# Kernel tuning notes

Measured on AMD Instinct MI355X. Metric: run time of the kernel, lower is better.

## Reference

```python
import jax, jax.numpy as jnp
from jax import lax
import numpy as np

EPS = 1e-5

def _quant(w):
    # BitNet-style binarization: sign(w) scaled by mean(|w|), with STE (identity grad)
    alpha = jnp.mean(jnp.abs(w))
    wq = jnp.sign(w) * alpha
    return w + lax.stop_gradient(wq - w)

def _bn(x, gamma, beta, axes):
    mean = jnp.mean(x, axis=axes, keepdims=True)
    var = jnp.var(x, axis=axes, keepdims=True)
    shape = [1] * x.ndim
    shape[1] = x.shape[1]
    return (x - mean) * lax.rsqrt(var + EPS) * gamma.reshape(shape) + beta.reshape(shape)

def _conv(x, w):
    return lax.conv_general_dilated(x, w, window_strides=(1, 1), padding=((1, 1), (1, 1)),
                                    dimension_numbers=('NCHW', 'OIHW', 'NCHW'))

def _maxpool2(x):
    return lax.reduce_window(x, -jnp.inf, lax.max, (1, 1, 2, 2), (1, 1, 2, 2), 'VALID')

def setup_inputs() -> dict:
    key = jax.random.key(0)
    ks = jax.random.split(key, 5)
    return {
        'x': jax.random.normal(ks[0], (1024, 3, 32, 32), jnp.float32),
        'w1': jax.random.normal(ks[1], (64, 3, 3, 3), jnp.float32) * 0.1,
        'g1': jnp.ones((64,), jnp.float32), 'b1': jnp.zeros((64,), jnp.float32),
        'w2': jax.random.normal(ks[2], (128, 64, 3, 3), jnp.float32) * 0.05,
        'g2': jnp.ones((128,), jnp.float32), 'b2': jnp.zeros((128,), jnp.float32),
        'wfc1': jax.random.normal(ks[3], (256, 8192), jnp.float32) * 0.02,
        'g3': jnp.ones((256,), jnp.float32), 'b3': jnp.zeros((256,), jnp.float32),
        'wfc2': jax.random.normal(ks[4], (10, 256), jnp.float32) * 0.1,
    }

def reference(x, w1, g1, b1, w2, g2, b2, wfc1, g3, b3, wfc2):
    h = _conv(x, _quant(w1))                 # [B,64,32,32]
    h = _maxpool2(jax.nn.relu(_bn(h, g1, b1, (0, 2, 3))))  # [B,64,16,16]
    h = _conv(h, _quant(w2))                 # [B,128,16,16]
    h = _maxpool2(jax.nn.relu(_bn(h, g2, b2, (0, 2, 3))))  # [B,128,8,8]
    h = h.reshape(h.shape[0], -1)            # [B,8192]
    h = h @ _quant(wfc1).T                   # [B,256]
    h = jax.nn.relu(_bn(h, g3, b3, (0,)))
    return h @ _quant(wfc2).T                # [B,10]
```

## Files before the change

kernel.cpp:

```cpp
#include <hip/hip_runtime.h>
#include <stdint.h>

typedef unsigned short u16;
typedef unsigned int u32;
typedef __attribute__((ext_vector_type(8))) short s8v;
typedef __attribute__((ext_vector_type(4))) float f4v;
typedef __attribute__((ext_vector_type(8))) u16 u16x8;
typedef __attribute__((ext_vector_type(4))) u16 u16x4;

__device__ __forceinline__ float bf2f(u16 u){
  union { u32 i; float f; } v; v.i = ((u32)u) << 16; return v.f;
}
__device__ __forceinline__ u16 f2bf(float f){
  union { float f; u32 i; } v; v.f = f;
  u32 i = v.i;
  return (u16)((i + 0x7fffu + ((i >> 16) & 1u)) >> 16);
}
__device__ __forceinline__ float sgnf(float w){
  return (w > 0.f) ? 1.f : ((w < 0.f) ? -1.f : 0.f);
}
__device__ __forceinline__ u16 sgn_bf(float w){
  return (w > 0.f) ? (u16)0x3F80 : ((w < 0.f) ? (u16)0xBF80 : (u16)0);
}

#define GLL16(gaddr, laddr) __builtin_amdgcn_global_load_lds( \
    (const __attribute__((address_space(1))) void*)(gaddr),   \
    (__attribute__((address_space(3))) void*)(laddr), 16, 0, 0)

__global__ __launch_bounds__(256) void k_gen(const float* __restrict__ w1, const float* __restrict__ w2,
                                             const float* __restrict__ wfc2, const float* __restrict__ wfc1,
                                             u16* __restrict__ qw1b, u16* __restrict__ qw2b,
                                             float* __restrict__ qwfc2, u16* __restrict__ qfc1b,
                                             float* __restrict__ partials){
  __shared__ u16 tile[128*72];
  int t = threadIdx.x;
  if (blockIdx.x < 306){
    int i = blockIdx.x * 256 + t;
    float av = 0.f; int slot;
    if (i < 73728){
      int j = i & 7, lane = (i >> 3) & 63, fid = i >> 9;
      int s = fid >> 4, ks = (fid >> 3) & 1, nt = fid & 7;
      int co = (lane & 15)*8 + nt;
      int c = ks*32 + (lane >> 4)*8 + j;
      float wv = w2[((size_t)co*64 + c)*9 + s];
      qw2b[i] = sgn_bf(wv);
      av = fabsf(wv); slot = 1;
    } else if (i < 73728 + 2048){
      int i3 = i - 73728;
      int j = i3 & 7, lane = (i3 >> 3) & 63, nt = i3 >> 9;
      int co = nt*16 + (lane & 15);
      int k = (lane >> 4)*8 + j;
      if (k < 27){
        float wv = w1[co*27 + k];
        qw1b[i3] = sgn_bf(wv);
        av = fabsf(wv);
      } else qw1b[i3] = (u16)0;
      slot = 0;
    } else {
      int i4 = i - (73728 + 2048);
      float wv = wfc2[i4];
      qwfc2[i4] = sgnf(wv);
      av = fabsf(wv); slot = 3;
    }
    #pragma unroll
    for (int off = 32; off > 0; off >>= 1) av += __shfl_xor(av, off);
    if ((t & 63) == 0) atomicAdd(partials + slot*256 + (blockIdx.x & 255), av);
  } else {
    int co = blockIdx.x - 306;
    const float4* src = (const float4*)(wfc1 + (size_t)co*8192);
    float av = 0.f;
    #pragma unroll
    for (int p = 0; p < 8; ++p){
      int k4 = t + p*256;
      float4 v = src[k4];
      int c = k4 >> 4, px = (k4 & 15)*4;
      u16* d = tile + c*72 + px;
      d[0] = sgn_bf(v.x); d[1] = sgn_bf(v.y); d[2] = sgn_bf(v.z); d[3] = sgn_bf(v.w);
      av += fabsf(v.x) + fabsf(v.y) + fabsf(v.z) + fabsf(v.w);
    }
    #pragma unroll
    for (int off = 32; off > 0; off >>= 1) av += __shfl_xor(av, off);
    if ((t & 63) == 0) atomicAdd(partials + 2*256 + (co & 255), av);
    __syncthreads();
    int co4 = co >> 4, co15 = co & 15;
    #pragma unroll
    for (int p = 0; p < 4; ++p){
      int m = t + p*256;
      int px = m >> 4, jj = m & 15;
      int kstep = px*4 + (jj >> 2), l16 = jj & 3;
      u16x8 o;
      #pragma unroll
      for (int u = 0; u < 8; ++u) o[u] = tile[(jj*8 + u)*72 + px];
      *(u16x8*)(qfc1b + ((size_t)(kstep*16 + co4)*512 + (l16*16 + co15)*8)) = o;
    }
  }
}

__global__ void k_red4(const float* __restrict__ partials, float* __restrict__ absum){
  int t = threadIdx.x, w = t >> 6, lane = t & 63;
  const float* p = partials + w*256;
  float s = p[lane] + p[lane + 64] + p[lane + 128] + p[lane + 192];
  #pragma unroll
  for (int off = 32; off > 0; off >>= 1) s += __shfl_xor(s, off);
  if (lane == 0) absum[w] = s;
}

__global__ __launch_bounds__(256) void k_conv1m(const float* __restrict__ x, const u16* __restrict__ qw1b,
                                                const float* __restrict__ absum, u16* __restrict__ p1raw,
                                                float* __restrict__ gs, float* __restrict__ gq){
  __shared__ __align__(8) u16 xs[3*34*36];
  __shared__ float ls1[64], ls2[64];
  int n = blockIdx.x, t = threadIdx.x;
  if (t < 64){ ls1[t] = 0.f; ls2[t] = 0.f; }
  for (int i = t; i < 1836; i += 256) ((u32*)xs)[i] = 0u;
  __syncthreads();
  const float4* xg = (const float4*)(x + (size_t)n * 3072);
  for (int i = t; i < 768; i += 256){
    float4 v = xg[i];
    int ci = i >> 8, rem = i & 255, y = rem >> 3, xq = (rem & 7) * 4;
    int base = ci*1224 + (y+1)*36 + 2 + xq;
    *(u32*)(xs + base)     = (u32)f2bf(v.x) | ((u32)f2bf(v.y) << 16);
    *(u32*)(xs + base + 2) = (u32)f2bf(v.z) | ((u32)f2bf(v.w) << 16);
  }
  int w = t >> 6, lane = t & 63, l15 = lane & 15, q = lane >> 4;
  int koff[8]; u32 kmsk[8];
  #pragma unroll
  for (int j = 0; j < 8; ++j){
    int k = q*8 + j;
    int d9 = (k*57) >> 9;
    int r9 = k - d9*9;
    int d3 = (r9*11) >> 5;
    int r3 = r9 - d3*3;
    koff[j] = d9*1224 + d3*36 + r3;
    kmsk[j] = (k < 27) ? 0xffffu : 0u;
  }
  const s8v* bp = (const s8v*)qw1b;
  s8v bf[4];
  #pragma unroll
  for (int nt = 0; nt < 4; ++nt) bf[nt] = bp[nt*64 + lane];
  float alpha = absum[0] * (1.f/1728.f);
  u16* p1img = p1raw + (size_t)n * 16384;
  float s1v[4], s2v[4];
  #pragma unroll
  for (int nt = 0; nt < 4; ++nt){ s1v[nt] = 0.f; s2v[nt] = 0.f; }
  __syncthreads();
  for (int chunk = 0; chunk < 4; ++chunk){
    #pragma unroll
    for (int i = 0; i < 4; ++i){
      int tl = w*4 + i;
      int r = tl*16 + l15;
      int g = (chunk*256 + r) >> 2, s = r & 3;
      int iy = 2*(g >> 4) + (s >> 1), ix = 2*(g & 15) + (s & 1);
      const u16* xb = xs + iy*36 + ix + 1;
      u32 pk2[4];
      #pragma unroll
      for (int kk = 0; kk < 4; ++kk){
        u32 lo = (u32)xb[koff[2*kk]]     & kmsk[2*kk];
        u32 hi = (u32)xb[koff[2*kk + 1]] & kmsk[2*kk + 1];
        pk2[kk] = lo | (hi << 16);
      }
      s8v av;
      ((u32*)&av)[0] = pk2[0]; ((u32*)&av)[1] = pk2[1];
      ((u32*)&av)[2] = pk2[2]; ((u32*)&av)[3] = pk2[3];
      int go = chunk*64 + tl*4 + q;
      u16* drow = p1img + go*64 + l15;
      #pragma unroll
      for (int nt = 0; nt < 4; ++nt){
        f4v c = (f4v)(0.0f);
        c = __builtin_amdgcn_mfma_f32_16x16x32_bf16(av, bf[nt], c, 0, 0, 0);
        s1v[nt] += c[0] + c[1] + c[2] + c[3];
        s2v[nt] += c[0]*c[0] + c[1]*c[1] + c[2]*c[2] + c[3]*c[3];
        float pm = fmaxf(fmaxf(c[0], c[1]), fmaxf(c[2], c[3]));
        drow[nt*16] = f2bf(pm * alpha);
      }
    }
  }
  #pragma unroll
  for (int nt = 0; nt < 4; ++nt){
    s1v[nt] += __shfl_xor(s1v[nt], 16); s1v[nt] += __shfl_xor(s1v[nt], 32);
    s2v[nt] += __shfl_xor(s2v[nt], 16); s2v[nt] += __shfl_xor(s2v[nt], 32);
  }
  if (q == 0){
    #pragma unroll
    for (int nt = 0; nt < 4; ++nt){
      atomicAdd(&ls1[nt*16 + l15], s1v[nt]);
      atomicAdd(&ls2[nt*16 + l15], s2v[nt]);
    }
  }
  __syncthreads();
  if (t < 64){
    atomicAdd(gs + t, ls1[t] * alpha);
    atomicAdd(gq + t, ls2[t] * alpha * alpha);
  }
}

__global__ __launch_bounds__(512, 4) void k_conv2m(const u16* __restrict__ p1raw, const u16* __restrict__ qw2b,
                                                   const float* __restrict__ absum,
                                                   const float* __restrict__ s1, const float* __restrict__ q1,
                                                   const float* __restrict__ g1, const float* __restrict__ b1,
                                                   u16* __restrict__ p2raw,
                                                   float* __restrict__ gs, float* __restrict__ gq){
  __shared__ __align__(16) u16 img[288*64];
  __shared__ __align__(16) u16 bstage[3][4096];
  int n = blockIdx.x, t = threadIdx.x;
  int c0 = (t & 7) * 8;
  float scv[8], biv[8];
  #pragma unroll
  for (int j = 0; j < 8; ++j){
    float m = s1[c0+j] * (1.f/1048576.f);
    float var = q1[c0+j] * (1.f/1048576.f) - m*m;
    float sc = g1[c0+j] * rsqrtf(var + 1e-5f);
    scv[j] = sc; biv[j] = b1[c0+j] - m*sc;
  }
  if (t < 256){
    int cl = t >> 7, y = (t >> 3) & 15, unit = t & 7;
    int px = y*18 + cl*17;
    int su = unit ^ (px & 7);
    *(u16x8*)(img + px*64 + su*8) = (u16x8)(u16)0;
  }
  const u16* src = p1raw + (size_t)n * 16384;
  #pragma unroll
  for (int i = 0; i < 4; ++i){
    int id = i*512 + t;
    int p0 = id >> 3, unit = id & 7;
    int y = p0 >> 4, xq = p0 & 15;
    int px = y*18 + xq + 1;
    int su = unit ^ (px & 7);
    u16x8 v = *(const u16x8*)(src + id*8);
    u16x8 o;
    #pragma unroll
    for (int j = 0; j < 8; ++j)
      o[j] = f2bf(fmaxf(bf2f(v[j]) * scv[j] + biv[j], 0.f));
    *(u16x8*)(img + px*64 + su*8) = o;
  }
  int w = t >> 6, lane = t & 63, l15 = lane & 15, q = lane >> 4;
  int wr = w >> 1, wc = w & 1;
  const char* bsrc = (const char*)qw2b;
  {
    const char* g = bsrc + w*1024 + lane*16;
    char* l = ((char*)bstage[0]) + w*1024;
    GLL16(g, l);
  }
  __syncthreads();
  f4v acc[4][4];
  #pragma unroll
  for (int a = 0; a < 4; ++a)
    #pragma unroll
    for (int b = 0; b < 4; ++b) acc[a][b] = (f4v)(0.0f);
  for (int p = 0; p < 18; ++p){
    int s = p >> 1, ks = p & 1;
    int dy = s / 3, dx = s - dy*3;
    if (p < 17){
      const char* g = bsrc + (size_t)(p + 1)*8192 + w*1024 + lane*16;
      char* l = ((char*)bstage[(p + 1) % 3]) + w*1024;
      GLL16(g, l);
      asm volatile("s_waitcnt vmcnt(1)" ::: "memory");
    } else {
      asm volatile("s_waitcnt vmcnt(0)" ::: "memory");
    }
    __builtin_amdgcn_s_barrier();
    asm volatile("" ::: "memory");
    const u16* bb = bstage[p % 3];
    s8v bf[4];
    #pragma unroll
    for (int nt = 0; nt < 4; ++nt) bf[nt] = *(const s8v*)(bb + ((wc*4 + nt)*64 + lane)*8);
    __builtin_amdgcn_s_setprio(1);
    #pragma unroll
    for (int mt = 0; mt < 4; ++mt){
      int yv = wr*4 + mt + dy - 1;
      if (yv >= 0 && yv <= 15){
        int px = yv*18 + l15 + dx;
        int su = (ks*4 + q) ^ (px & 7);
        s8v av = *(const s8v*)(img + px*64 + su*8);
        #pragma unroll
        for (int nt = 0; nt < 4; ++nt)
          acc[mt][nt] = __builtin_amdgcn_mfma_f32_16x16x32_bf16(av, bf[nt], acc[mt][nt], 0, 0, 0);
      }
    }
    __builtin_amdgcn_s_setprio(0);
  }
  float alpha = absum[1] * (1.f/73728.f);
  float s1v[4], s2v[4];
  #pragma unroll
  for (int nt = 0; nt < 4; ++nt){ s1v[nt] = 0.f; s2v[nt] = 0.f; }
  #pragma unroll
  for (int mp = 0; mp < 2; ++mp){
    #pragma unroll
    for (int rp = 0; rp < 2; ++rp){
      u16x4 pk;
      #pragma unroll
      for (int nt = 0; nt < 4; ++nt){
        float v0 = acc[2*mp][nt][2*rp]     * alpha;
        float v1 = acc[2*mp][nt][2*rp+1]   * alpha;
        float v2 = acc[2*mp+1][nt][2*rp]   * alpha;
        float v3 = acc[2*mp+1][nt][2*rp+1] * alpha;
        s1v[nt] += v0 + v1 + v2 + v3;
        s2v[nt] += v0*v0 + v1*v1 + v2*v2 + v3*v3;
        pk[nt] = f2bf(fmaxf(fmaxf(v0, v1), fmaxf(v2, v3)));
      }
      int opx = (wr*2 + mp)*8 + (q*2 + rp);
      *(u16x4*)(p2raw + ((size_t)n*64 + opx)*128 + l15*8 + wc*4) = pk;
    }
  }
  #pragma unroll
  for (int nt = 0; nt < 4; ++nt){
    s1v[nt] += __shfl_xor(s1v[nt], 16); s1v[nt] += __shfl_xor(s1v[nt], 32);
    s2v[nt] += __shfl_xor(s2v[nt], 16); s2v[nt] += __shfl_xor(s2v[nt], 32);
  }
  __syncthreads();
  float* ls = (float*)img;
  if (t < 256) ls[t] = 0.f;
  __syncthreads();
  if (q == 0){
    #pragma unroll
    for (int nt = 0; nt < 4; ++nt){
      atomicAdd(&ls[l15*8 + wc*4 + nt], s1v[nt]);
      atomicAdd(&ls[128 + l15*8 + wc*4 + nt], s2v[nt]);
    }
  }
  __syncthreads();
  if (t < 128){ atomicAdd(gs + t, ls[t]); atomicAdd(gq + t, ls[128 + t]); }
}

__global__ __launch_bounds__(256) void k_bn2(u16* __restrict__ p2,
                                             const float* __restrict__ s2, const float* __restrict__ q2,
                                             const float* __restrict__ g2, const float* __restrict__ b2){
  size_t i = (size_t)blockIdx.x * 256 + threadIdx.x;
  int c0 = ((int)(i & 15)) * 8;
  float scv[8], biv[8];
  #pragma unroll
  for (int j = 0; j < 8; ++j){
    float m = s2[c0+j] * (1.f/262144.f);
    float var = q2[c0+j] * (1.f/262144.f) - m*m;
    float sc = g2[c0+j] * rsqrtf(var + 1e-5f);
    scv[j] = sc; biv[j] = b2[c0+j] - m*sc;
  }
  u16x8 v = *(u16x8*)(p2 + i*8);
  u16x8 o;
  #pragma unroll
  for (int j = 0; j < 8; ++j)
    o[j] = f2bf(fmaxf(bf2f(v[j]) * scv[j] + biv[j], 0.f));
  *(u16x8*)(p2 + i*8) = o;
}

__global__ __launch_bounds__(256) void k_fc1m(const u16* __restrict__ p2, const u16* __restrict__ qfc1b,
                                              const float* __restrict__ absum, float* __restrict__ h3p){
  int t = threadIdx.x;
  int bm = blockIdx.x, bn = blockIdx.y, kb = blockIdx.z;
  int w = t >> 6, lane = t & 63, l15 = lane & 15, q = lane >> 4;
  int rowbase = bm*128 + (w >> 1)*64;
  int ntb = bn*8 + (w & 1)*4;
  const s8v* bp = (const s8v*)qfc1b;
  f4v acc[4][4];
  #pragma unroll
  for (int a = 0; a < 4; ++a)
    #pragma unroll
    for (int b = 0; b < 4; ++b) acc[a][b] = (f4v)(0.0f);
  #pragma unroll 2
  for (int ks = 0; ks < 16; ++ks){
    int kst = kb*16 + ks;
    s8v bf[4], af[4];
    #pragma unroll
    for (int nt = 0; nt < 4; ++nt) bf[nt] = bp[(kst*16 + ntb + nt)*64 + lane];
    #pragma unroll
    for (int mt = 0; mt < 4; ++mt)
      af[mt] = *(const s8v*)(p2 + (size_t)(rowbase + mt*16 + l15)*8192 + kst*32 + q*8);
    #pragma unroll
    for (int mt = 0; mt < 4; ++mt)
      #pragma unroll
      for (int nt = 0; nt < 4; ++nt)
        acc[mt][nt] = __builtin_amdgcn_mfma_f32_16x16x32_bf16(af[mt], bf[nt], acc[mt][nt], 0, 0, 0);
  }
  float alpha = absum[2] * (1.f/2097152.f);
  float* dst = h3p + (size_t)kb * 262144;
  #pragma unroll
  for (int mt = 0; mt < 4; ++mt)
    #pragma unroll
    for (int nt = 0; nt < 4; ++nt){
      int col = (ntb + nt)*16 + l15;
      #pragma unroll
      for (int r = 0; r < 4; ++r)
        dst[(size_t)(rowbase + mt*16 + q*4 + r)*256 + col] = acc[mt][nt][r] * alpha;
    }
}

__global__ __launch_bounds__(256) void k_fin3f(const float* __restrict__ h3p, float* __restrict__ h3,
                                               float* __restrict__ s3, float* __restrict__ q3){
  int jb = blockIdx.x, ns = blockIdx.y, t = threadIdx.x;
  int jj = t & 31, nn = t >> 5;
  int j = jb*32 + jj;
  float s1 = 0.f, s2 = 0.f;
  #pragma unroll
  for (int i = 0; i < 2; ++i){
    int n = ns*16 + i*8 + nn;
    float v = 0.f;
    #pragma unroll
    for (int kb = 0; kb < 16; ++kb) v += h3p[(size_t)kb*262144 + n*256 + j];
    h3[n*256 + j] = v;
    s1 += v; s2 += v*v;
  }
  __shared__ float l1[256], l2[256];
  l1[t] = s1; l2[t] = s2;
  __syncthreads();
  if (t < 32){
    float a = 0.f, b = 0.f;
    #pragma unroll
    for (int k = 0; k < 8; ++k){ a += l1[t+32*k]; b += l2[t+32*k]; }
    atomicAdd(s3 + jb*32 + t, a); atomicAdd(q3 + jb*32 + t, b);
  }
}

__global__ __launch_bounds__(64) void k_fc2(const float* __restrict__ h3, const float* __restrict__ qwfc2,
                                            const float* __restrict__ absum,
                                            const float* __restrict__ s3, const float* __restrict__ q3,
                                            const float* __restrict__ g3, const float* __restrict__ b3,
                                            float* __restrict__ out){
  int n = blockIdx.x, lane = threadIdx.x;
  float a[4];
  #pragma unroll
  for (int i = 0; i < 4; ++i){
    int j = lane + 64*i;
    float m = s3[j] * (1.f/1024.f);
    float var = q3[j] * (1.f/1024.f) - m*m;
    float sc = g3[j] * rsqrtf(var + 1e-5f);
    float v = h3[(size_t)n*256 + j] * sc + (b3[j] - m*sc);
    a[i] = fmaxf(v, 0.f);
  }
  float alpha = absum[3] * (1.f/2560.f);
  #pragma unroll
  for (int k = 0; k < 10; ++k){
    float p = 0.f;
    #pragma unroll
    for (int i = 0; i < 4; ++i) p += a[i] * qwfc2[k*256 + lane + 64*i];
    #pragma unroll
    for (int off = 32; off > 0; off >>= 1) p += __shfl_down(p, off);
    if (lane == 0) out[n*10 + k] = p * alpha;
  }
}

extern "C" void kernel_launch(void* const* d_in, const int* in_sizes, int n_in,
                              void* d_out, int out_size, void* d_ws, size_t ws_size,
                              hipStream_t stream){
  (void)in_sizes; (void)n_in; (void)out_size; (void)ws_size;
  const float* x    = (const float*)d_in[0];
  const float* w1   = (const float*)d_in[1];
  const float* g1   = (const float*)d_in[2];
  const float* b1   = (const float*)d_in[3];
  const float* w2   = (const float*)d_in[4];
  const float* g2   = (const float*)d_in[5];
  const float* b2   = (const float*)d_in[6];
  const float* wfc1 = (const float*)d_in[7];
  const float* g3   = (const float*)d_in[8];
  const float* b3   = (const float*)d_in[9];
  const float* wfc2 = (const float*)d_in[10];
  float* out = (float*)d_out;

  float* wsf = (float*)d_ws;
  char*  wsb = (char*)d_ws;
  float* absum = wsf;
  float* s1 = wsf + 16;   float* q1 = wsf + 80;
  float* s2 = wsf + 144;  float* q2 = wsf + 272;
  float* s3 = wsf + 1024; float* q3 = wsf + 1280;
  float* partials = wsf + 2048;
  u16*   qw1b  = (u16*)(wsf + 4096);
  u16*   qw2b  = (u16*)(wsb + (64u << 10));
  float* qwfc2 = (float*)(wsb + (256u << 10));
  float* h3    = (float*)(wsb + (1ull << 20));
  u16*   qfc1b = (u16*)(wsb + (2ull << 20));
  u16*   p1t   = (u16*)(wsb + (8ull << 20) + 4096);
  u16*   p2    = (u16*)(wsb + (112ull << 20));
  float* h3p   = (float*)(wsb + (128ull << 20));

  hipMemsetAsync(wsf, 0, 3072 * sizeof(float), stream);
  k_gen<<<562, 256, 0, stream>>>(w1, w2, wfc2, wfc1, qw1b, qw2b, qwfc2, qfc1b, partials);
  k_red4<<<1, 256, 0, stream>>>(partials, absum);
  k_conv1m<<<1024, 256, 0, stream>>>(x, qw1b, absum, p1t, s1, q1);
  k_conv2m<<<1024, 512, 0, stream>>>(p1t, qw2b, absum, s1, q1, g1, b1, p2, s2, q2);
  k_bn2<<<4096, 256, 0, stream>>>(p2, s2, q2, g2, b2);
  k_fc1m<<<dim3(8, 2, 16), 256, 0, stream>>>(p2, qfc1b, absum, h3p);
  k_fin3f<<<dim3(8, 64), 256, 0, stream>>>(h3p, h3, s3, q3);
  k_fc2<<<1024, 64, 0, stream>>>(h3, qwfc2, absum, s3, q3, g3, b3, out);
}
```

Before: 220.4 us.

## Fuse BN2+ReLU into FC1 A-operand load and retile FC1 grid

Removes the standalone k_bn2 pass, which read and wrote the pooled conv2 activations in place. FC1 now applies the per-channel BN scale/bias and ReLU to each A fragment as it is loaded, with the scale and bias for a given channel group computed once per ks4 iteration. FC1 is also retiled: each wave now computes 16 rows instead of 64, the grid becomes 32x2x8 with K split into 8 chunks instead of 16, and k_fin3f sums 8 partials. This saves a full activation round trip and a launch. In exchange each block streams more of the B matrix per row, repeats the BN math on every A load, and the split-K loop visits K steps in a strided order.

```diff
diff --git a/kernel.cpp b/kernel.cpp
--- a/kernel.cpp
+++ b/kernel.cpp
@@ -238,8 +238,7 @@
   const char* bsrc = (const char*)qw2b;
   {
     const char* g = bsrc + w*1024 + lane*16;
-    char* l = ((char*)bstage[0]) + w*1024;
-    GLL16(g, l);
+    GLL16(g, ((char*)bstage[0]) + w*1024);
   }
   __syncthreads();
   f4v acc[4][4];
@@ -252,8 +251,7 @@
     int dy = s / 3, dx = s - dy*3;
     if (p < 17){
       const char* g = bsrc + (size_t)(p + 1)*8192 + w*1024 + lane*16;
-      char* l = ((char*)bstage[(p + 1) % 3]) + w*1024;
-      GLL16(g, l);
+      GLL16(g, ((char*)bstage[(p + 1) % 3]) + w*1024);
       asm volatile("s_waitcnt vmcnt(1)" ::: "memory");
     } else {
       asm volatile("s_waitcnt vmcnt(0)" ::: "memory");
@@ -322,66 +320,60 @@
   if (t < 128){ atomicAdd(gs + t, ls[t]); atomicAdd(gq + t, ls[128 + t]); }
 }
 
-__global__ __launch_bounds__(256) void k_bn2(u16* __restrict__ p2,
-                                             const float* __restrict__ s2, const float* __restrict__ q2,
-                                             const float* __restrict__ g2, const float* __restrict__ b2){
-  size_t i = (size_t)blockIdx.x * 256 + threadIdx.x;
-  int c0 = ((int)(i & 15)) * 8;
-  float scv[8], biv[8];
-  #pragma unroll
-  for (int j = 0; j < 8; ++j){
-    float m = s2[c0+j] * (1.f/262144.f);
-    float var = q2[c0+j] * (1.f/262144.f) - m*m;
-    float sc = g2[c0+j] * rsqrtf(var + 1e-5f);
-    scv[j] = sc; biv[j] = b2[c0+j] - m*sc;
-  }
-  u16x8 v = *(u16x8*)(p2 + i*8);
-  u16x8 o;
-  #pragma unroll
-  for (int j = 0; j < 8; ++j)
-    o[j] = f2bf(fmaxf(bf2f(v[j]) * scv[j] + biv[j], 0.f));
-  *(u16x8*)(p2 + i*8) = o;
-}
-
 __global__ __launch_bounds__(256) void k_fc1m(const u16* __restrict__ p2, const u16* __restrict__ qfc1b,
-                                              const float* __restrict__ absum, float* __restrict__ h3p){
+                                              const float* __restrict__ absum,
+                                              const float* __restrict__ s2, const float* __restrict__ q2,
+                                              const float* __restrict__ g2, const float* __restrict__ b2,
+                                              float* __restrict__ h3p){
   int t = threadIdx.x;
   int bm = blockIdx.x, bn = blockIdx.y, kb = blockIdx.z;
   int w = t >> 6, lane = t & 63, l15 = lane & 15, q = lane >> 4;
-  int rowbase = bm*128 + (w >> 1)*64;
-  int ntb = bn*8 + (w & 1)*4;
+  int wr = w >> 1, wc = w & 1;
+  int rowbase = bm*32 + wr*16;
+  int ntb = bn*8 + wc*4;
   const s8v* bp = (const s8v*)qfc1b;
-  f4v acc[4][4];
-  #pragma unroll
-  for (int a = 0; a < 4; ++a)
-    #pragma unroll
-    for (int b = 0; b < 4; ++b) acc[a][b] = (f4v)(0.0f);
-  #pragma unroll 2
-  for (int ks = 0; ks < 16; ++ks){
-    int kst = kb*16 + ks;
-    s8v bf[4], af[4];
-    #pragma unroll
-    for (int nt = 0; nt < 4; ++nt) bf[nt] = bp[(kst*16 + ntb + nt)*64 + lane];
-    #pragma unroll
-    for (int mt = 0; mt < 4; ++mt)
-      af[mt] = *(const s8v*)(p2 + (size_t)(rowbase + mt*16 + l15)*8192 + kst*32 + q*8);
-    #pragma unroll
-    for (int mt = 0; mt < 4; ++mt)
+  f4v acc[4];
+  #pragma unroll
+  for (int b = 0; b < 4; ++b) acc[b] = (f4v)(0.0f);
+  #pragma unroll
+  for (int ks4 = 0; ks4 < 4; ++ks4){
+    int c0 = ks4*32 + q*8;
+    float scv[8], biv[8];
+    #pragma unroll
+    for (int j = 0; j < 8; ++j){
+      float m = s2[c0+j] * (1.f/262144.f);
+      float var = q2[c0+j] * (1.f/262144.f) - m*m;
+      float sc = g2[c0+j] * rsqrtf(var + 1e-5f);
+      scv[j] = sc; biv[j] = b2[c0+j] - m*sc;
+    }
+    #pragma unroll 2
+    for (int u = 0; u < 8; ++u){
+      int ks = ks4 + u*4;
+      int kst = kb*32 + ks;
+      s8v bf[4];
+      #pragma unroll
+      for (int nt = 0; nt < 4; ++nt) bf[nt] = bp[(kst*16 + ntb + nt)*64 + lane];
+      u16x8 araw = *(const u16x8*)(p2 + (size_t)(rowbase + l15)*8192 + kst*32 + q*8);
+      s8v av;
+      #pragma unroll
+      for (int j = 0; j < 8; ++j){
+        float f = fmaxf(bf2f(araw[j]) * scv[j] + biv[j], 0.f);
+        ((u16*)&av)[j] = f2bf(f);
+      }
       #pragma unroll
       for (int nt = 0; nt < 4; ++nt)
-        acc[mt][nt] = __builtin_amdgcn_mfma_f32_16x16x32_bf16(af[mt], bf[nt], acc[mt][nt], 0, 0, 0);
+        acc[nt] = __builtin_amdgcn_mfma_f32_16x16x32_bf16(av, bf[nt], acc[nt], 0, 0, 0);
+    }
   }
   float alpha = absum[2] * (1.f/2097152.f);
   float* dst = h3p + (size_t)kb * 262144;
   #pragma unroll
-  for (int mt = 0; mt < 4; ++mt)
-    #pragma unroll
-    for (int nt = 0; nt < 4; ++nt){
-      int col = (ntb + nt)*16 + l15;
-      #pragma unroll
-      for (int r = 0; r < 4; ++r)
-        dst[(size_t)(rowbase + mt*16 + q*4 + r)*256 + col] = acc[mt][nt][r] * alpha;
-    }
+  for (int nt = 0; nt < 4; ++nt){
+    int col = (ntb + nt)*16 + l15;
+    #pragma unroll
+    for (int r = 0; r < 4; ++r)
+      dst[(size_t)(rowbase + q*4 + r)*256 + col] = acc[nt][r] * alpha;
+  }
 }
 
 __global__ __launch_bounds__(256) void k_fin3f(const float* __restrict__ h3p, float* __restrict__ h3,
@@ -395,7 +387,7 @@
     int n = ns*16 + i*8 + nn;
     float v = 0.f;
     #pragma unroll
-    for (int kb = 0; kb < 16; ++kb) v += h3p[(size_t)kb*262144 + n*256 + j];
+    for (int kb = 0; kb < 8; ++kb) v += h3p[(size_t)kb*262144 + n*256 + j];
     h3[n*256 + j] = v;
     s1 += v; s2 += v*v;
   }
@@ -476,8 +468,7 @@
   k_red4<<<1, 256, 0, stream>>>(partials, absum);
   k_conv1m<<<1024, 256, 0, stream>>>(x, qw1b, absum, p1t, s1, q1);
   k_conv2m<<<1024, 512, 0, stream>>>(p1t, qw2b, absum, s1, q1, g1, b1, p2, s2, q2);
-  k_bn2<<<4096, 256, 0, stream>>>(p2, s2, q2, g2, b2);
-  k_fc1m<<<dim3(8, 2, 16), 256, 0, stream>>>(p2, qfc1b, absum, h3p);
+  k_fc1m<<<dim3(32, 2, 8), 256, 0, stream>>>(p2, qfc1b, absum, s2, q2, g2, b2, h3p);
   k_fin3f<<<dim3(8, 64), 256, 0, stream>>>(h3p, h3, s3, q3);
   k_fc2<<<1024, 64, 0, stream>>>(h3, qwfc2, absum, s3, q3, g3, b3, out);
 }
```

Measured after the change: 215.8 us. -2.1%, faster.
